# Optimization experiments

Measured on AMD Instinct MI355X. Metric: run time of the kernel, lower is better.

## Reference

```python
import jax, jax.numpy as jnp
import numpy as np

N_TOKENS = 65536   # number of embeddings to quantize
CODE_DIM = 768     # embedding dim
NUM_CODES = 4096   # codebook size


def setup_inputs() -> dict:
    key = jax.random.key(0)
    k1, k2 = jax.random.split(key)
    x = jax.random.normal(k1, (N_TOKENS, CODE_DIM), dtype=jnp.float32)
    codebook = jax.random.normal(k2, (NUM_CODES, CODE_DIM), dtype=jnp.float32)
    return {"x": x, "codebook": codebook}


def reference(x, codebook):
    # argmin over squared distances == argmin over cdist (sqrt is monotone).
    x2 = jnp.sum(x * x, axis=-1, keepdims=True)          # [N, 1]
    c2 = jnp.sum(codebook * codebook, axis=-1)           # [K]
    dist = x2 + c2[None, :] - 2.0 * jnp.einsum('nd,kd->nk', x, codebook)  # [N, K]
    indices = jnp.argmin(dist, axis=-1)                  # [N] int
    quantized = codebook[indices]                        # gather [N, D]
    # straight-through estimator: forward = quantized, grad flows to x
    q_ste = x + jax.lax.stop_gradient(quantized - x)
    return q_ste, indices
```

## Files before the change

kernel.cpp:

```cpp
#include <hip/hip_runtime.h>

#define N_TOKENS  65536
#define CODE_DIM  768
#define NUM_CODES 4096

#define MARGIN 0.05f
#define FLTMAX 3.4028235e38f

typedef __attribute__((ext_vector_type(8))) short bf16x8;
typedef __attribute__((ext_vector_type(4))) float f32x4;

__device__ __forceinline__ unsigned short f2bf(float f) {
  unsigned int u = __float_as_uint(f);
  unsigned int r = (u + 0x7fffu + ((u >> 16) & 1u)) >> 16;
  return (unsigned short)r;
}
__device__ __forceinline__ float bf2f(unsigned short h) {
  return __uint_as_float(((unsigned int)h) << 16);
}
__device__ __forceinline__ void gl2lds16(const void* g, void* l) {
  __builtin_amdgcn_global_load_lds(
      (const __attribute__((address_space(1))) unsigned int*)g,
      (__attribute__((address_space(3))) unsigned int*)l, 16, 0, 0);
}

__global__ __launch_bounds__(256) void vq_convert_kernel(
    const float* __restrict__ x, const float* __restrict__ cb,
    unsigned short* __restrict__ xh, unsigned short* __restrict__ xl,
    unsigned short* __restrict__ cbh, unsigned short* __restrict__ cbl,
    float* __restrict__ x2, float* __restrict__ c2, int* __restrict__ fcnt) {
  if (blockIdx.x == 0 && threadIdx.x == 0) *fcnt = 0;
  const int wave = threadIdx.x >> 6;
  const int lane = threadIdx.x & 63;
  const int row  = blockIdx.x * 4 + wave;
  const float* src;
  unsigned short *hdst, *ldst;
  float* ndst;
  if (row < N_TOKENS) {
    src = x + (size_t)row * CODE_DIM;
    hdst = xh + (size_t)row * CODE_DIM;
    ldst = xl + (size_t)row * CODE_DIM;
    ndst = x2 + row;
  } else {
    const int r = row - N_TOKENS;
    if (r >= NUM_CODES) return;
    src = cb + (size_t)r * CODE_DIM;
    hdst = cbh + (size_t)r * CODE_DIM;
    ldst = cbl + (size_t)r * CODE_DIM;
    ndst = c2 + r;
  }
  const float4* s4 = (const float4*)src;
  ushort4* h4 = (ushort4*)hdst;
  ushort4* l4 = (ushort4*)ldst;
  float acc = 0.f;
#pragma unroll
  for (int i = 0; i < 3; ++i) {
    float4 f = s4[lane + 64 * i];
    ushort4 h, l;
    h.x = f2bf(f.x); l.x = f2bf(f.x - bf2f(h.x));
    h.y = f2bf(f.y); l.y = f2bf(f.y - bf2f(h.y));
    h.z = f2bf(f.z); l.z = f2bf(f.z - bf2f(h.z));
    h.w = f2bf(f.w); l.w = f2bf(f.w - bf2f(h.w));
    h4[lane + 64 * i] = h;
    l4[lane + 64 * i] = l;
    acc += (f.x * f.x + f.y * f.y) + (f.z * f.z + f.w * f.w);
  }
#pragma unroll
  for (int off = 32; off > 0; off >>= 1) acc += __shfl_down(acc, off, 64);
  if (lane == 0) *ndst = acc;
}

__global__ __launch_bounds__(256, 2) void vq_mfma_kernel(
    const unsigned short* __restrict__ xh, const unsigned short* __restrict__ xl,
    const unsigned short* __restrict__ cbh, const unsigned short* __restrict__ cbl,
    const float* __restrict__ c2, int* __restrict__ out_idx,
    int* __restrict__ fcnt, int* __restrict__ flist) {
  __shared__ unsigned short sAh[4096], sAl[4096], sBh[4096], sBl[4096];
  __shared__ float redv[256], redsv[256];
  __shared__ int   redi[256];

  const int tid = threadIdx.x;
  const int wave = tid >> 6, lane = tid & 63;
  const int l15 = lane & 15, quad = lane >> 4;
  const int wr = wave >> 1, wc = wave & 1;
  const int tokBase = blockIdx.x * 128;

  const int chunk0 = wave * 128 + lane;
  const int chunk1 = chunk0 + 64;
  const int r0 = chunk0 >> 2, c0 = (chunk0 & 3) * 8;
  const int r1 = chunk1 >> 2, c1 = (chunk1 & 3) * 8;
  const size_t aoffg0 = (size_t)(tokBase + r0) * CODE_DIM + c0;
  const size_t aoffg1 = (size_t)(tokBase + r1) * CODE_DIM + c1;
  const size_t boffg0 = (size_t)r0 * CODE_DIM + c0;
  const size_t boffg1 = (size_t)r1 * CODE_DIM + c1;
  unsigned short* ldsA0 = &sAh[wave * 1024];
  unsigned short* ldsA1 = &sAh[wave * 1024 + 512];
  unsigned short* ldsAl0 = &sAl[wave * 1024];
  unsigned short* ldsAl1 = &sAl[wave * 1024 + 512];
  unsigned short* ldsB0 = &sBh[wave * 1024];
  unsigned short* ldsB1 = &sBh[wave * 1024 + 512];
  unsigned short* ldsBl0 = &sBl[wave * 1024];
  unsigned short* ldsBl1 = &sBl[wave * 1024 + 512];

  const int aoffL = (wr * 64 + l15) * 32 + quad * 8;
  const int boffL = (wc * 64 + l15) * 32 + quad * 8;

  float v[4][4], sv[4][4];
  int bi[4][4];
#pragma unroll
  for (int i = 0; i < 4; ++i)
#pragma unroll
    for (int r = 0; r < 4; ++r) { v[i][r] = FLTMAX; sv[i][r] = FLTMAX; bi[i][r] = 0; }

  for (int kt = 0; kt < NUM_CODES / 128; ++kt) {
    const int kbase = kt * 128;
    const size_t kb768 = (size_t)kbase * CODE_DIM;
    f32x4 acc[4][4];
#pragma unroll
    for (int i = 0; i < 4; ++i)
#pragma unroll
      for (int j = 0; j < 4; ++j) acc[i][j] = (f32x4){0.f, 0.f, 0.f, 0.f};

    for (int ks = 0; ks < CODE_DIM / 32; ++ks) {
      const int k0 = ks * 32;
      __syncthreads();
      gl2lds16(xh + aoffg0 + k0, ldsA0);
      gl2lds16(xh + aoffg1 + k0, ldsA1);
      gl2lds16(xl + aoffg0 + k0, ldsAl0);
      gl2lds16(xl + aoffg1 + k0, ldsAl1);
      gl2lds16(cbh + boffg0 + kb768 + k0, ldsB0);
      gl2lds16(cbh + boffg1 + kb768 + k0, ldsB1);
      gl2lds16(cbl + boffg0 + kb768 + k0, ldsBl0);
      gl2lds16(cbl + boffg1 + kb768 + k0, ldsBl1);
      __syncthreads();

      bf16x8 fah[4], fal[4], fbh[4], fbl[4];
#pragma unroll
      for (int i = 0; i < 4; ++i) {
        fah[i] = *(const bf16x8*)&sAh[aoffL + i * 512];
        fal[i] = *(const bf16x8*)&sAl[aoffL + i * 512];
      }
#pragma unroll
      for (int j = 0; j < 4; ++j) {
        fbh[j] = *(const bf16x8*)&sBh[boffL + j * 512];
        fbl[j] = *(const bf16x8*)&sBl[boffL + j * 512];
      }
#pragma unroll
      for (int i = 0; i < 4; ++i)
#pragma unroll
        for (int j = 0; j < 4; ++j) {
          acc[i][j] = __builtin_amdgcn_mfma_f32_16x16x32_bf16(fah[i], fbh[j], acc[i][j], 0, 0, 0);
          acc[i][j] = __builtin_amdgcn_mfma_f32_16x16x32_bf16(fah[i], fbl[j], acc[i][j], 0, 0, 0);
          acc[i][j] = __builtin_amdgcn_mfma_f32_16x16x32_bf16(fal[i], fbh[j], acc[i][j], 0, 0, 0);
        }
    }

#pragma unroll
    for (int j = 0; j < 4; ++j) {
      const int kcol = kbase + wc * 64 + j * 16 + l15;
      const float c2j = c2[kcol];
#pragma unroll
      for (int i = 0; i < 4; ++i)
#pragma unroll
        for (int r = 0; r < 4; ++r) {
          float s = fmaf(-2.0f, acc[i][j][r], c2j);
          float vo = v[i][r];
          sv[i][r] = fminf(sv[i][r], fmaxf(s, vo));
          bool lt = s < vo;
          v[i][r]  = lt ? s : vo;
          bi[i][r] = lt ? kcol : bi[i][r];
        }
    }
  }

#pragma unroll
  for (int i = 0; i < 4; ++i)
#pragma unroll
    for (int r = 0; r < 4; ++r) {
      float vv = v[i][r], svv = sv[i][r];
      int ii = bi[i][r];
#pragma unroll
      for (int m = 1; m < 16; m <<= 1) {
        float ov = __shfl_xor(vv, m, 64);
        float osv = __shfl_xor(svv, m, 64);
        int oi = __shfl_xor(ii, m, 64);
        float nsv = fminf(fminf(svv, osv), fmaxf(vv, ov));
        bool take = (ov < vv) || (ov == vv && oi < ii);
        vv = take ? ov : vv;
        ii = take ? oi : ii;
        svv = nsv;
      }
      if (l15 == 0) {
        int row = wr * 64 + i * 16 + quad * 4 + r;
        redv[row * 2 + wc] = vv;
        redsv[row * 2 + wc] = svv;
        redi[row * 2 + wc] = ii;
      }
    }
  __syncthreads();
  if (tid < 128) {
    float v0 = redv[tid * 2], v1 = redv[tid * 2 + 1];
    float s0 = redsv[tid * 2], s1 = redsv[tid * 2 + 1];
    int i0 = redi[tid * 2], i1 = redi[tid * 2 + 1];
    bool take = (v1 < v0) || (v1 == v0 && i1 < i0);
    float bv = take ? v1 : v0;
    int bidx = take ? i1 : i0;
    float bsv = fminf(fminf(s0, s1), fmaxf(v0, v1));
    out_idx[tokBase + tid] = bidx;
    if (bsv - bv < MARGIN) {
      int p = atomicAdd(fcnt, 1);
      flist[p] = tokBase + tid;
    }
  }
}

__global__ __launch_bounds__(256) void vq_rescan_kernel(
    const float* __restrict__ x, const float* __restrict__ cb,
    const float* __restrict__ x2, const float* __restrict__ c2,
    const int* __restrict__ fcnt, const int* __restrict__ flist,
    int* __restrict__ out_idx) {
  __shared__ float xs[CODE_DIM];
  __shared__ float rv[256];
  __shared__ int ri[256];
  const int nf = *fcnt;
  for (int f = blockIdx.x; f < nf; f += gridDim.x) {
    const int tok = flist[f];
    __syncthreads();
    if (threadIdx.x < 192)
      ((float4*)xs)[threadIdx.x] = ((const float4*)(x + (size_t)tok * CODE_DIM))[threadIdx.x];
    __syncthreads();
    const float xx = x2[tok];
    float bv = FLTMAX;
    int bidx = 0;
    for (int kk = 0; kk < NUM_CODES / 256; ++kk) {
      const int k = kk * 256 + threadIdx.x;
      const float4* crow = (const float4*)(cb + (size_t)k * CODE_DIM);
      float acc = 0.f;
      for (int c = 0; c < CODE_DIM / 4; ++c) {
        float4 cv = crow[c];
        float4 xv = ((float4*)xs)[c];
        acc += (xv.x * cv.x + xv.y * cv.y) + (xv.z * cv.z + xv.w * cv.w);
      }
      float dist = (xx + c2[k]) - 2.0f * acc;
      if (dist < bv) { bv = dist; bidx = k; }
    }
    rv[threadIdx.x] = bv;
    ri[threadIdx.x] = bidx;
    __syncthreads();
    for (int s = 128; s > 0; s >>= 1) {
      if (threadIdx.x < s) {
        float ov = rv[threadIdx.x + s];
        int oi = ri[threadIdx.x + s];
        if (ov < rv[threadIdx.x] || (ov == rv[threadIdx.x] && oi < ri[threadIdx.x])) {
          rv[threadIdx.x] = ov;
          ri[threadIdx.x] = oi;
        }
      }
      __syncthreads();
    }
    if (threadIdx.x == 0) out_idx[tok] = ri[0];
  }
}

__global__ __launch_bounds__(256) void vq_gather_kernel(
    const float* __restrict__ cb, const int* __restrict__ idx,
    float* __restrict__ out) {
  const int wave = threadIdx.x >> 6;
  const int lane = threadIdx.x & 63;
  const int token = blockIdx.x * 4 + wave;
  const int k = idx[token];
  const float4* src = (const float4*)(cb + (size_t)k * CODE_DIM);
  float4* dst = (float4*)(out + (size_t)token * CODE_DIM);
#pragma unroll
  for (int i = 0; i < 3; ++i) dst[lane + 64 * i] = src[lane + 64 * i];
  if (lane == 0) out[(size_t)N_TOKENS * CODE_DIM + token] = (float)k;
}

#define MT 64
#define KT 128
#define DT 32
#define LDSTRIDE 36

__global__ __launch_bounds__(256) void vq_norms_kernel(
    const float* __restrict__ x, const float* __restrict__ cb,
    float* __restrict__ x2, float* __restrict__ c2) {
  const int wave = threadIdx.x >> 6;
  const int lane = threadIdx.x & 63;
  const int row = blockIdx.x * 4 + wave;
  const float* src;
  float* dst;
  if (row < N_TOKENS) {
    src = x + (size_t)row * CODE_DIM;
    dst = x2 + row;
  } else {
    const int r = row - N_TOKENS;
    if (r >= NUM_CODES) return;
    src = cb + (size_t)r * CODE_DIM;
    dst = c2 + r;
  }
  const float4* s4 = (const float4*)src;
  float acc = 0.f;
#pragma unroll
  for (int i = 0; i < 3; ++i) {
    float4 vv = s4[lane + 64 * i];
    acc += (vv.x * vv.x + vv.y * vv.y) + (vv.z * vv.z + vv.w * vv.w);
  }
#pragma unroll
  for (int off = 32; off > 0; off >>= 1) acc += __shfl_down(acc, off, 64);
  if (lane == 0) *dst = acc;
}

__global__ __launch_bounds__(256) void vq_argmin_kernel(
    const float* __restrict__ x, const float* __restrict__ cb,
    const float* __restrict__ x2, const float* __restrict__ c2,
    int* __restrict__ out_idx) {
  __shared__ float xs[MT * LDSTRIDE];
  __shared__ float cs[KT * LDSTRIDE];
  __shared__ float x2s[MT];
  __shared__ float c2s[KT];
  const int tid = threadIdx.x;
  const int tx = tid & 15;
  const int ty = tid >> 4;
  const int tokBase = blockIdx.x * MT;
  if (tid < MT) x2s[tid] = x2[tokBase + tid];
  float bestv[4];
  int besti[4];
#pragma unroll
  for (int i = 0; i < 4; ++i) { bestv[i] = FLTMAX; besti[i] = 0; }
  const float4* xg = (const float4*)x;
  const float4* cg = (const float4*)cb;
  for (int kt = 0; kt < NUM_CODES / KT; ++kt) {
    const int kBase = kt * KT;
    __syncthreads();
    if (tid < KT) c2s[tid] = c2[kBase + tid];
    float acc[4][8];
#pragma unroll
    for (int i = 0; i < 4; ++i)
#pragma unroll
      for (int j = 0; j < 8; ++j) acc[i][j] = 0.f;
    for (int dc = 0; dc < CODE_DIM / DT; ++dc) {
      __syncthreads();
#pragma unroll
      for (int r = 0; r < 2; ++r) {
        int fidx = tid + 256 * r;
        int row = fidx >> 3, c4 = fidx & 7;
        float4 vv = xg[(size_t)(tokBase + row) * (CODE_DIM / 4) + dc * 8 + c4];
        *(float4*)&xs[row * LDSTRIDE + c4 * 4] = vv;
      }
#pragma unroll
      for (int r = 0; r < 4; ++r) {
        int fidx = tid + 256 * r;
        int row = fidx >> 3, c4 = fidx & 7;
        float4 vv = cg[(size_t)(kBase + row) * (CODE_DIM / 4) + dc * 8 + c4];
        *(float4*)&cs[row * LDSTRIDE + c4 * 4] = vv;
      }
      __syncthreads();
#pragma unroll
      for (int dd = 0; dd < DT / 4; ++dd) {
        float4 xv[4], cv[8];
#pragma unroll
        for (int i = 0; i < 4; ++i)
          xv[i] = *(const float4*)&xs[(ty + 16 * i) * LDSTRIDE + dd * 4];
#pragma unroll
        for (int j = 0; j < 8; ++j)
          cv[j] = *(const float4*)&cs[(tx + 16 * j) * LDSTRIDE + dd * 4];
#pragma unroll
        for (int i = 0; i < 4; ++i)
#pragma unroll
          for (int j = 0; j < 8; ++j)
            acc[i][j] += (xv[i].x * cv[j].x + xv[i].y * cv[j].y) +
                         (xv[i].z * cv[j].z + xv[i].w * cv[j].w);
      }
    }
#pragma unroll
    for (int i = 0; i < 4; ++i) {
      const float xx = x2s[ty + 16 * i];
#pragma unroll
      for (int j = 0; j < 8; ++j) {
        float dist = (xx + c2s[tx + 16 * j]) - 2.0f * acc[i][j];
        int k = kBase + tx + 16 * j;
        if (dist < bestv[i]) { bestv[i] = dist; besti[i] = k; }
      }
    }
  }
  __syncthreads();
  float* rdv = xs;
  int* rdi = (int*)cs;
#pragma unroll
  for (int i = 0; i < 4; ++i) {
    const int m = ty + 16 * i;
    rdv[m * 16 + tx] = bestv[i];
    rdi[m * 16 + tx] = besti[i];
  }
  __syncthreads();
  if (tid < MT) {
    float bv = rdv[tid * 16];
    int bidx = rdi[tid * 16];
#pragma unroll
    for (int t = 1; t < 16; ++t) {
      float vv = rdv[tid * 16 + t];
      int kk = rdi[tid * 16 + t];
      if (vv < bv || (vv == bv && kk < bidx)) { bv = vv; bidx = kk; }
    }
    out_idx[tokBase + tid] = bidx;
  }
}

extern "C" void kernel_launch(void* const* d_in, const int* in_sizes, int n_in,
                              void* d_out, int out_size, void* d_ws, size_t ws_size,
                              hipStream_t stream) {
  (void)in_sizes; (void)n_in; (void)out_size;
  const float* x = (const float*)d_in[0];
  const float* cb = (const float*)d_in[1];
  float* out = (float*)d_out;

  char* w = (char*)d_ws;
  unsigned short* xh = (unsigned short*)w;  w += (size_t)N_TOKENS * CODE_DIM * 2;
  unsigned short* xl = (unsigned short*)w;  w += (size_t)N_TOKENS * CODE_DIM * 2;
  unsigned short* cbh = (unsigned short*)w; w += (size_t)NUM_CODES * CODE_DIM * 2;
  unsigned short* cbl = (unsigned short*)w; w += (size_t)NUM_CODES * CODE_DIM * 2;
  float* x2 = (float*)w;  w += (size_t)N_TOKENS * 4;
  float* c2 = (float*)w;  w += (size_t)NUM_CODES * 4;
  int* idx = (int*)w;     w += (size_t)N_TOKENS * 4;
  int* flist = (int*)w;   w += (size_t)N_TOKENS * 4;
  int* fcnt = (int*)w;    w += 256;
  const size_t need = (size_t)(w - (char*)d_ws);

  if (ws_size >= need) {
    vq_convert_kernel<<<(N_TOKENS + NUM_CODES) / 4, 256, 0, stream>>>(
        x, cb, xh, xl, cbh, cbl, x2, c2, fcnt);
    vq_mfma_kernel<<<N_TOKENS / 128, 256, 0, stream>>>(
        xh, xl, cbh, cbl, c2, idx, fcnt, flist);
    vq_rescan_kernel<<<512, 256, 0, stream>>>(x, cb, x2, c2, fcnt, flist, idx);
    vq_gather_kernel<<<N_TOKENS / 4, 256, 0, stream>>>(cb, idx, out);
  } else {
    float* fx2 = (float*)d_ws;
    float* fc2 = fx2 + N_TOKENS;
    int* fidx = (int*)(fc2 + NUM_CODES);
    vq_norms_kernel<<<(N_TOKENS + NUM_CODES + 3) / 4, 256, 0, stream>>>(x, cb, fx2, fc2);
    vq_argmin_kernel<<<N_TOKENS / MT, 256, 0, stream>>>(x, cb, fx2, fc2, fidx);
    vq_gather_kernel<<<N_TOKENS / 4, 256, 0, stream>>>(cb, fidx, out);
  }
}
```

Baseline: 2.081 ms.

## Double K-step tile to 64 with XOR-swizzled LDS layout and tighter fallback margin

Raises the per-iteration K slice from 32 to 64, which halves the number of barrier pairs and global-to-LDS load rounds per code tile. LDS rows are now 64 elements wide and use an XOR swizzle on 16-byte chunks so the fragment reads avoid bank conflicts. The ambiguity MARGIN drops from 0.05 to 0.006, so fewer tokens are sent to the exact fp32 recheck. The trade-offs are doubled LDS usage, which may affect occupancy at 2 blocks per CU, and a tighter margin that relies on the split-bf16 error staying small.

```diff
diff --git a/kernel.cpp b/kernel.cpp
--- a/kernel.cpp
+++ b/kernel.cpp
@@ -4,7 +4,7 @@
 #define CODE_DIM  768
 #define NUM_CODES 4096
 
-#define MARGIN 0.05f
+#define MARGIN 0.006f
 #define FLTMAX 3.4028235e38f
 
 typedef __attribute__((ext_vector_type(8))) short bf16x8;
@@ -75,7 +75,7 @@
     const unsigned short* __restrict__ cbh, const unsigned short* __restrict__ cbl,
     const float* __restrict__ c2, int* __restrict__ out_idx,
     int* __restrict__ fcnt, int* __restrict__ flist) {
-  __shared__ unsigned short sAh[4096], sAl[4096], sBh[4096], sBl[4096];
+  __shared__ unsigned short sAh[8192], sAl[8192], sBh[8192], sBl[8192];
   __shared__ float redv[256], redsv[256];
   __shared__ int   redi[256];
 
@@ -85,25 +85,14 @@
   const int wr = wave >> 1, wc = wave & 1;
   const int tokBase = blockIdx.x * 128;
 
-  const int chunk0 = wave * 128 + lane;
-  const int chunk1 = chunk0 + 64;
-  const int r0 = chunk0 >> 2, c0 = (chunk0 & 3) * 8;
-  const int r1 = chunk1 >> 2, c1 = (chunk1 & 3) * 8;
-  const size_t aoffg0 = (size_t)(tokBase + r0) * CODE_DIM + c0;
-  const size_t aoffg1 = (size_t)(tokBase + r1) * CODE_DIM + c1;
-  const size_t boffg0 = (size_t)r0 * CODE_DIM + c0;
-  const size_t boffg1 = (size_t)r1 * CODE_DIM + c1;
-  unsigned short* ldsA0 = &sAh[wave * 1024];
-  unsigned short* ldsA1 = &sAh[wave * 1024 + 512];
-  unsigned short* ldsAl0 = &sAl[wave * 1024];
-  unsigned short* ldsAl1 = &sAl[wave * 1024 + 512];
-  unsigned short* ldsB0 = &sBh[wave * 1024];
-  unsigned short* ldsB1 = &sBh[wave * 1024 + 512];
-  unsigned short* ldsBl0 = &sBl[wave * 1024];
-  unsigned short* ldsBl1 = &sBl[wave * 1024 + 512];
-
-  const int aoffL = (wr * 64 + l15) * 32 + quad * 8;
-  const int boffL = (wc * 64 + l15) * 32 + quad * 8;
+  const int lr = lane >> 3;
+  const int cSrc = (lane & 7) ^ (lr & 7);
+  const size_t aOff = (size_t)(tokBase + wave * 32 + lr) * CODE_DIM + cSrc * 8;
+  const size_t bOff = (size_t)(wave * 32 + lr) * CODE_DIM + cSrc * 8;
+
+  const int swz = l15 & 7;
+  const int arow = (wr * 64 + l15) * 64;
+  const int brow = (wc * 64 + l15) * 64;
 
   float v[4][4], sv[4][4];
   int bi[4][4];
@@ -114,45 +103,51 @@
 
   for (int kt = 0; kt < NUM_CODES / 128; ++kt) {
     const int kbase = kt * 128;
-    const size_t kb768 = (size_t)kbase * CODE_DIM;
+    const size_t kb = (size_t)kbase * CODE_DIM;
     f32x4 acc[4][4];
 #pragma unroll
     for (int i = 0; i < 4; ++i)
 #pragma unroll
       for (int j = 0; j < 4; ++j) acc[i][j] = (f32x4){0.f, 0.f, 0.f, 0.f};
 
-    for (int ks = 0; ks < CODE_DIM / 32; ++ks) {
-      const int k0 = ks * 32;
+    for (int ks = 0; ks < CODE_DIM / 64; ++ks) {
+      const int k0 = ks * 64;
       __syncthreads();
-      gl2lds16(xh + aoffg0 + k0, ldsA0);
-      gl2lds16(xh + aoffg1 + k0, ldsA1);
-      gl2lds16(xl + aoffg0 + k0, ldsAl0);
-      gl2lds16(xl + aoffg1 + k0, ldsAl1);
-      gl2lds16(cbh + boffg0 + kb768 + k0, ldsB0);
-      gl2lds16(cbh + boffg1 + kb768 + k0, ldsB1);
-      gl2lds16(cbl + boffg0 + kb768 + k0, ldsBl0);
-      gl2lds16(cbl + boffg1 + kb768 + k0, ldsBl1);
+#pragma unroll
+      for (int t = 0; t < 4; ++t) {
+        const size_t ga = aOff + t * (8 * CODE_DIM) + k0;
+        const size_t gb = bOff + kb + t * (8 * CODE_DIM) + k0;
+        const int ld = wave * 2048 + t * 512;
+        gl2lds16(xh + ga, &sAh[ld]);
+        gl2lds16(xl + ga, &sAl[ld]);
+        gl2lds16(cbh + gb, &sBh[ld]);
+        gl2lds16(cbl + gb, &sBl[ld]);
+      }
       __syncthreads();
 
-      bf16x8 fah[4], fal[4], fbh[4], fbl[4];
-#pragma unroll
-      for (int i = 0; i < 4; ++i) {
-        fah[i] = *(const bf16x8*)&sAh[aoffL + i * 512];
-        fal[i] = *(const bf16x8*)&sAl[aoffL + i * 512];
-      }
-#pragma unroll
-      for (int j = 0; j < 4; ++j) {
-        fbh[j] = *(const bf16x8*)&sBh[boffL + j * 512];
-        fbl[j] = *(const bf16x8*)&sBl[boffL + j * 512];
-      }
-#pragma unroll
-      for (int i = 0; i < 4; ++i)
+#pragma unroll
+      for (int ks2 = 0; ks2 < 2; ++ks2) {
+        const int coffq = ((ks2 * 4 + quad) ^ swz) * 8;
+        bf16x8 fah[4], fal[4], fbh[4], fbl[4];
+#pragma unroll
+        for (int i = 0; i < 4; ++i) {
+          fah[i] = *(const bf16x8*)&sAh[arow + i * 1024 + coffq];
+          fal[i] = *(const bf16x8*)&sAl[arow + i * 1024 + coffq];
+        }
 #pragma unroll
         for (int j = 0; j < 4; ++j) {
-          acc[i][j] = __builtin_amdgcn_mfma_f32_16x16x32_bf16(fah[i], fbh[j], acc[i][j], 0, 0, 0);
-          acc[i][j] = __builtin_amdgcn_mfma_f32_16x16x32_bf16(fah[i], fbl[j], acc[i][j], 0, 0, 0);
-          acc[i][j] = __builtin_amdgcn_mfma_f32_16x16x32_bf16(fal[i], fbh[j], acc[i][j], 0, 0, 0);
+          fbh[j] = *(const bf16x8*)&sBh[brow + j * 1024 + coffq];
+          fbl[j] = *(const bf16x8*)&sBl[brow + j * 1024 + coffq];
         }
+#pragma unroll
+        for (int i = 0; i < 4; ++i)
+#pragma unroll
+          for (int j = 0; j < 4; ++j) {
+            acc[i][j] = __builtin_amdgcn_mfma_f32_16x16x32_bf16(fah[i], fbh[j], acc[i][j], 0, 0, 0);
+            acc[i][j] = __builtin_amdgcn_mfma_f32_16x16x32_bf16(fah[i], fbl[j], acc[i][j], 0, 0, 0);
+            acc[i][j] = __builtin_amdgcn_mfma_f32_16x16x32_bf16(fal[i], fbh[j], acc[i][j], 0, 0, 0);
+          }
+      }
     }
 
 #pragma unroll
```

New measurement: 1.744 ms. 16.2% less time.
